# Kernel optimization log

Measured on AMD Instinct MI355X. Metric: run time of the kernel, lower is better.

The kernel has to match this reference:

```python
import jax, jax.numpy as jnp
import numpy as np

H, W = 64, 64          # self.shape = (W, H) = (64, 64)
REG_MAX = 16
TOPK = 4

def _dwconv(y, w, b):
    # y: (N, L, C) -> depthwise 3x3 conv on (N, C, H, W) -> (N, L, C)
    N, L, C = y.shape
    img = jnp.transpose(y, (0, 2, 1)).reshape(N, C, H, W)
    out = jax.lax.conv_general_dilated(
        img, w, (1, 1), ((1, 1), (1, 1)),
        dimension_numbers=('NCHW', 'OIHW', 'NCHW'), feature_group_count=C)
    out = out + b[None, :, None, None]
    return jnp.transpose(out.reshape(N, C, H * W), (0, 2, 1))

def _mlp(x, fc1_w, fc1_b, dw1_w, dw1_b, fc2_w, fc2_b, dw2_w, dw2_b, fc3_w, fc3_b):
    h = x @ fc1_w.T + fc1_b
    h = jax.nn.gelu(_dwconv(h, dw1_w, dw1_b), approximate=False)  # torch nn.GELU is exact erf
    h = h @ fc2_w.T + fc2_b
    h = jax.nn.gelu(_dwconv(h, dw2_w, dw2_b), approximate=False)
    return h @ fc3_w.T + fc3_b

def setup_inputs() -> dict:
    key = jax.random.key(0)
    ks = iter(jax.random.split(key, 16))
    d = {}
    d['x'] = jax.random.normal(next(ks), (1, 32, H * W, 256), dtype=jnp.float32)
    for p in ('c_', 'r_'):
        out3 = 1 if p == 'c_' else 4 * (REG_MAX + 1)
        d[p + 'fc1_w'] = 0.02 * jax.random.normal(next(ks), (256, 256), dtype=jnp.float32)
        d[p + 'fc1_b'] = jnp.zeros((256,), jnp.float32)
        d[p + 'dw1_w'] = 0.3 * jax.random.normal(next(ks), (256, 1, 3, 3), dtype=jnp.float32)
        d[p + 'dw1_b'] = jnp.zeros((256,), jnp.float32)
        d[p + 'fc2_w'] = 0.02 * jax.random.normal(next(ks), (256, 256), dtype=jnp.float32)
        d[p + 'fc2_b'] = jnp.zeros((256,), jnp.float32)
        d[p + 'dw2_w'] = 0.3 * jax.random.normal(next(ks), (256, 1, 3, 3), dtype=jnp.float32)
        d[p + 'dw2_b'] = jnp.zeros((256,), jnp.float32)
        d[p + 'fc3_w'] = 0.02 * jax.random.normal(next(ks), (out3, 256), dtype=jnp.float32)
        d[p + 'fc3_b'] = jnp.zeros((out3,), jnp.float32)
    d['rc1_w'] = 0.1 * jax.random.normal(next(ks), (64, 4 * (TOPK + 1)), dtype=jnp.float32)
    d['rc1_b'] = jnp.zeros((64,), jnp.float32)
    d['rc2_w'] = 0.1 * jax.random.normal(next(ks), (1, 64), dtype=jnp.float32)
    d['rc2_b'] = jnp.zeros((1,), jnp.float32)
    return d

def reference(x,
              c_fc1_w, c_fc1_b, c_dw1_w, c_dw1_b, c_fc2_w, c_fc2_b, c_dw2_w, c_dw2_b, c_fc3_w, c_fc3_b,
              r_fc1_w, r_fc1_b, r_dw1_w, r_dw1_b, r_fc2_w, r_fc2_b, r_dw2_w, r_dw2_b, r_fc3_w, r_fc3_b,
              rc1_w, rc1_b, rc2_w, rc2_b):
    xs = x[0]                                   # (N, L, C)
    N = xs.shape[0]
    reg_pred = _mlp(xs, r_fc1_w, r_fc1_b, r_dw1_w, r_dw1_b, r_fc2_w, r_fc2_b,
                    r_dw2_w, r_dw2_b, r_fc3_w, r_fc3_b)  # (N, L, 4*(reg_max+1))
    prob = jax.nn.softmax(
        jnp.transpose(reg_pred, (0, 2, 1)).reshape(N, 4, REG_MAX + 1, H, W), axis=2)
    pt = jnp.transpose(prob, (0, 1, 3, 4, 2))   # (N,4,H,W,reg_max+1)
    topk, _ = jax.lax.top_k(pt, TOPK)           # (N,4,H,W,topk), sorted desc like torch
    stat = jnp.concatenate([topk, topk.mean(axis=-1, keepdims=True)], axis=-1)
    stat = jnp.transpose(stat, (0, 1, 4, 2, 3)).reshape(N, 4 * (TOPK + 1), H, W)
    q = jax.nn.relu(jnp.einsum('nchw,oc->nohw', stat, rc1_w) + rc1_b[None, :, None, None])
    q = jax.nn.sigmoid(jnp.einsum('nchw,oc->nohw', q, rc2_w) + rc2_b[None, :, None, None])
    cls = _mlp(xs, c_fc1_w, c_fc1_b, c_dw1_w, c_dw1_b, c_fc2_w, c_fc2_b,
               c_dw2_w, c_dw2_b, c_fc3_w, c_fc3_b)      # (N, L, 1)
    cls = jax.nn.sigmoid(jnp.transpose(cls, (0, 2, 1)).reshape(N, 1, H, W)) * q
    proj = jnp.arange(REG_MAX + 1, dtype=reg_pred.dtype)  # linspace(0, reg_max, reg_max+1)
    dist = jax.nn.softmax(reg_pred.reshape(-1, REG_MAX + 1), axis=1) @ proj
    boxes = dist.reshape(N, H, W, 4) / REG_MAX
    return cls, boxes, reg_pred.reshape(N, H, W, 4 * (REG_MAX + 1))
```

## Files before the change

### kernel.cpp

```cpp
#include <hip/hip_runtime.h>
#include <hip/hip_bf16.h>

typedef __bf16 bf16x8 __attribute__((ext_vector_type(8)));
typedef float f32x4 __attribute__((ext_vector_type(4)));
typedef float f32x2 __attribute__((ext_vector_type(2)));

__device__ __forceinline__ float bf2f(unsigned short b) {
  unsigned int u = ((unsigned int)b) << 16;
  return __builtin_bit_cast(float, u);
}
__device__ __forceinline__ unsigned short f2bf(float f) {
  unsigned int u = __builtin_bit_cast(unsigned int, f);
  unsigned int r = u + 0x7fffu + ((u >> 16) & 1u);
  return (unsigned short)(r >> 16);
}
__device__ __forceinline__ f32x2 unpack2(unsigned int u) {
  f32x2 r;
  r.x = __builtin_bit_cast(float, u << 16);
  r.y = __builtin_bit_cast(float, u & 0xffff0000u);
  return r;
}

__device__ __forceinline__ void gload16(const void* g, void* l) {
  typedef __attribute__((address_space(1))) const void* gp_t;
  typedef __attribute__((address_space(3))) void* lp_t;
  __builtin_amdgcn_global_load_lds((gp_t)g, (lp_t)l, 16, 0, 0);
}

__device__ __forceinline__ f32x2 gelu2(f32x2 x) {
  f32x2 m = x * x;
  f32x2 t = m * (-0.10295273f) + (-2.3021967f);
  f32x2 u = x * t;
  f32x2 e;
  e.x = __builtin_amdgcn_exp2f(u.x);
  e.y = __builtin_amdgcn_exp2f(u.y);
  f32x2 d = e + 1.0f;
  f32x2 r;
  r.x = __builtin_amdgcn_rcpf(d.x);
  r.y = __builtin_amdgcn_rcpf(d.y);
  return x * r;
}
__device__ __forceinline__ unsigned int cvt_pk_bf16(float lo, float hi) {
  unsigned int r;
  asm("v_cvt_pk_bf16_f32 %0, %1, %2" : "=v"(r) : "v"(lo), "v"(hi));
  return r;
}

__global__ __launch_bounds__(256) void cvt_x(const float* __restrict__ in,
                                             unsigned short* __restrict__ out) {
  long i = ((long)blockIdx.x * 256 + threadIdx.x) * 8;
  float4 a = *(const float4*)(in + i);
  float4 b = *(const float4*)(in + i + 4);
  __align__(16) unsigned short o[8];
  o[0] = f2bf(a.x); o[1] = f2bf(a.y); o[2] = f2bf(a.z); o[3] = f2bf(a.w);
  o[4] = f2bf(b.x); o[5] = f2bf(b.y); o[6] = f2bf(b.z); o[7] = f2bf(b.w);
  *(uint4*)(out + i) = *(uint4*)o;
}

__global__ __launch_bounds__(256) void prep_all(
    const float* __restrict__ c1w, const float* __restrict__ r1w,
    const float* __restrict__ c2w, const float* __restrict__ r2w,
    const float* __restrict__ c3w, const float* __restrict__ r3w, const float* __restrict__ r3b,
    const float* __restrict__ c1b, const float* __restrict__ r1b,
    const float* __restrict__ c2b, const float* __restrict__ r2b,
    const float* __restrict__ d1wc, const float* __restrict__ d1bc,
    const float* __restrict__ d1wr, const float* __restrict__ d1br,
    const float* __restrict__ d2wc, const float* __restrict__ d2bc,
    const float* __restrict__ d2wr, const float* __restrict__ d2br,
    unsigned short* __restrict__ w1cat, unsigned short* __restrict__ w2cat,
    unsigned short* __restrict__ c3wb, unsigned short* __restrict__ wr3pad,
    float* __restrict__ br3pad, float* __restrict__ b1cat, float* __restrict__ b2cat,
    float* __restrict__ wd1, float* __restrict__ bd1,
    float* __restrict__ wd2, float* __restrict__ bd2) {
  int i = blockIdx.x * 256 + threadIdx.x;
  {
    int which = i >> 16, j = i & 65535;
    float v = (which == 0) ? c1w[j] : (which == 1) ? r1w[j] : (which == 2) ? c2w[j] : r2w[j];
    unsigned short* dst = (which < 2) ? (w1cat + which * 65536) : (w2cat + (which - 2) * 65536);
    dst[j] = f2bf(v);
  }
  if (i < 32768) {
    int r = i >> 8, c = i & 255;
    wr3pad[i] = (r < 68) ? f2bf(r3w[r * 256 + c]) : (unsigned short)0;
    if (i < 128) br3pad[i] = (i < 68) ? r3b[i] : 0.f;
  }
  if (i < 256) c3wb[i] = f2bf(c3w[i]);
  if (i < 4608) {
    int tap = i >> 9, ch = i & 511, cc = ch & 255;
    wd1[i] = (ch < 256) ? d1wc[cc * 9 + tap] : d1wr[cc * 9 + tap];
    wd2[i] = (ch < 256) ? d2wc[cc * 9 + tap] : d2wr[cc * 9 + tap];
  }
  if (i < 512) {
    bd1[i] = (i < 256) ? d1bc[i] : d1br[i & 255];
    bd2[i] = (i < 256) ? d2bc[i] : d2br[i & 255];
    b1cat[i] = (i < 256) ? c1b[i] : r1b[i & 255];
    b2cat[i] = (i < 256) ? c2b[i] : r2b[i & 255];
  }
}

__global__ __launch_bounds__(256, 4) void gemm_glds(
    const unsigned short* __restrict__ A, int lda, int zAoff,
    const unsigned short* __restrict__ W, int zWoff,
    const float* __restrict__ bias, int zBoff,
    unsigned short* __restrict__ Out, int ldo, int zOoff, int lnN,
    float* __restrict__ OutF) {
  __shared__ unsigned short lds[2][8192];
  const int z = blockIdx.z;
  const unsigned short* Az = A + (long)z * zAoff;
  const unsigned short* Wz = W + (long)z * zWoff;
  const float* biasz = bias + z * zBoff;
  unsigned short* Outz = Out + (long)z * zOoff;

  const int nwg = gridDim.x;
  const int bid = blockIdx.x;
  const int wg = (bid & 7) * (nwg >> 3) + (bid >> 3);
  const int mtile = wg >> lnN;
  const int ntile = wg & ((1 << lnN) - 1);
  const long row0 = (long)mtile * 128;
  const int col0 = ntile * 128;

  const int tid = threadIdx.x;
  const int lane = tid & 63;
  const int wid = tid >> 6;
  const int wr = (wid >> 1) * 64;
  const int wc = (wid & 1) * 64;
  const int rr = lane & 15;
  const int gk = lane >> 4;
  const int swz = (rr >> 1) & 3;

  const int srow_l = (wid << 4) + (lane >> 2);
  const int sgl = lane & 3;

  f32x4 acc[4][4] = {};

  auto stage = [&](int buf, int k0) {
    #pragma unroll
    for (int j = 0; j < 4; j++) {
      const int slotbase = j * 256 + (wid << 6);
      unsigned short* ldst = &lds[buf][slotbase * 8];
      const int row = (j & 1) * 64 + srow_l;
      const int g = sgl ^ ((row >> 1) & 3);
      const unsigned short* src;
      if (j < 2) src = Az + (row0 + row) * (long)lda + k0 + g * 8;
      else       src = Wz + (long)(col0 + row) * 256 + k0 + g * 8;
      gload16(src, ldst);
    }
  };

  stage(0, 0);
  #pragma unroll
  for (int ks = 0; ks < 8; ks++) {
    if (ks < 7) {
      stage((ks + 1) & 1, (ks + 1) * 32);
      asm volatile("s_waitcnt vmcnt(4)" ::: "memory");
    } else {
      asm volatile("s_waitcnt vmcnt(0)" ::: "memory");
    }
    __builtin_amdgcn_s_barrier();
    asm volatile("" ::: "memory");
    const unsigned short* buf = lds[ks & 1];
    bf16x8 af[4], bf[4];
    #pragma unroll
    for (int mi = 0; mi < 4; mi++)
      af[mi] = __builtin_bit_cast(bf16x8,
          *(const uint4*)&buf[(wr + mi * 16 + rr) * 32 + ((gk ^ swz) * 8)]);
    #pragma unroll
    for (int ni = 0; ni < 4; ni++)
      bf[ni] = __builtin_bit_cast(bf16x8,
          *(const uint4*)&buf[4096 + (wc + ni * 16 + rr) * 32 + ((gk ^ swz) * 8)]);
    #pragma unroll
    for (int mi = 0; mi < 4; mi++)
      #pragma unroll
      for (int ni = 0; ni < 4; ni++)
        acc[mi][ni] = __builtin_amdgcn_mfma_f32_16x16x32_bf16(af[mi], bf[ni], acc[mi][ni], 0, 0, 0);
    asm volatile("" ::: "memory");
    __builtin_amdgcn_s_barrier();
  }

  #pragma unroll
  for (int mi = 0; mi < 4; mi++) {
    const int rbase = wr + mi * 16 + (lane >> 4) * 4;
    #pragma unroll
    for (int ni = 0; ni < 4; ni++) {
      const int c_ = wc + ni * 16 + (lane & 15);
      const float bv = biasz[col0 + c_];
      #pragma unroll
      for (int r = 0; r < 4; r++) {
        const float val = acc[mi][ni][r] + bv;
        Outz[(row0 + rbase + r) * (long)ldo + col0 + c_] = f2bf(val);
        if (OutF != nullptr && c_ < 68)
          OutF[(row0 + rbase + r) * 68L + c_] = val;
      }
    }
  }
}

template <bool CLS>
__global__ __launch_bounds__(256) void dwconv_gelu4(
    const unsigned short* __restrict__ In,
    const float* __restrict__ Wt, const float* __restrict__ Bt,
    unsigned short* __restrict__ Out,
    const unsigned short* __restrict__ Wc3, const float* __restrict__ bc3,
    float* __restrict__ cls_logit) {
  const int t = blockIdx.x * 256 + threadIdx.x;
  const int g = t & 63;
  const int p = t >> 6;
  const int n = p >> 10;
  const int h = (p >> 4) & 63;
  const int w0 = (p & 15) << 2;
  const int cbase = g << 3;
  f32x2 acc[4][4];
  {
    float4 b0 = *(const float4*)(Bt + cbase);
    float4 b1 = *(const float4*)(Bt + cbase + 4);
    f32x2 bb[4];
    bb[0].x = b0.x; bb[0].y = b0.y; bb[1].x = b0.z; bb[1].y = b0.w;
    bb[2].x = b1.x; bb[2].y = b1.y; bb[3].x = b1.z; bb[3].y = b1.w;
    #pragma unroll
    for (int k = 0; k < 4; k++)
      #pragma unroll
      for (int i = 0; i < 4; i++) acc[k][i] = bb[i];
  }
  #pragma unroll
  for (int dy = -1; dy <= 1; dy++) {
    const int hh = h + dy;
    if (hh < 0 || hh > 63) continue;
    const float* wbase = Wt + ((dy + 1) * 3) * 512 + cbase;
    f32x2 wt[3][4];
    #pragma unroll
    for (int j = 0; j < 3; j++) {
      float4 a0 = *(const float4*)(wbase + j * 512);
      float4 a1 = *(const float4*)(wbase + j * 512 + 4);
      wt[j][0].x = a0.x; wt[j][0].y = a0.y; wt[j][1].x = a0.z; wt[j][1].y = a0.w;
      wt[j][2].x = a1.x; wt[j][2].y = a1.y; wt[j][3].x = a1.z; wt[j][3].y = a1.w;
    }
    const long rowtok = (long)(((n << 6) + hh) << 6);
    f32x2 f[6][4];
    #pragma unroll
    for (int d = 0; d < 6; d++) {
      const int col = w0 - 1 + d;
      uint4 v = {0u, 0u, 0u, 0u};
      if (col >= 0 && col < 64)
        v = *(const uint4*)(In + (rowtok + col) * 512 + cbase);
      f[d][0] = unpack2(v.x); f[d][1] = unpack2(v.y);
      f[d][2] = unpack2(v.z); f[d][3] = unpack2(v.w);
    }
    #pragma unroll
    for (int k = 0; k < 4; k++)
      #pragma unroll
      for (int j = 0; j < 3; j++)
        #pragma unroll
        for (int i = 0; i < 4; i++)
          acc[k][i] += f[k + j][i] * wt[j][i];
  }
  f32x2 w3[4];
  if (CLS) {
    const int cc = cbase & 255;
    uint4 wv = *(const uint4*)(Wc3 + cc);
    w3[0] = unpack2(wv.x); w3[1] = unpack2(wv.y);
    w3[2] = unpack2(wv.z); w3[3] = unpack2(wv.w);
  }
  const long mbase = ((long)((n << 6) + h) << 6) + w0;
  float s[4];
  #pragma unroll
  for (int k = 0; k < 4; k++) {
    __align__(16) unsigned int ov[4];
    f32x2 ge[4];
    #pragma unroll
    for (int i = 0; i < 4; i++) {
      ge[i] = gelu2(acc[k][i]);
      ov[i] = cvt_pk_bf16(ge[i].x, ge[i].y);
    }
    if (!CLS || cbase >= 256)
      *(uint4*)(Out + (mbase + k) * 512 + cbase) = *(uint4*)ov;
    if (CLS) {
      f32x2 sp = ge[0] * w3[0] + ge[1] * w3[1] + ge[2] * w3[2] + ge[3] * w3[3];
      s[k] = sp.x + sp.y;
    }
  }
  if (CLS) {
    #pragma unroll
    for (int k = 0; k < 4; k++) {
      #pragma unroll
      for (int m = 16; m >= 1; m >>= 1) s[k] += __shfl_xor(s[k], m);
    }
    if (g == 0) {
      float b = bc3[0];
      float4 o;
      o.x = s[0] + b; o.y = s[1] + b; o.z = s[2] + b; o.w = s[3] + b;
      *(float4*)(cls_logit + mbase) = o;
    }
  }
}

__global__ __launch_bounds__(256) void post_kernel(
    const unsigned short* __restrict__ RP,
    const float* __restrict__ cls_logit,
    const float* __restrict__ rc1_w, const float* __restrict__ rc1_b,
    const float* __restrict__ rc2_w, const float* __restrict__ rc2_b,
    float* __restrict__ out_cls, float* __restrict__ out_boxes) {
  int m = blockIdx.x * 256 + threadIdx.x;
  const unsigned short* rp = RP + (long)m * 128;
  __align__(16) unsigned short raw[72];
  #pragma unroll
  for (int q = 0; q < 9; q++)
    *(uint4*)(raw + q * 8) = *(const uint4*)(rp + q * 8);
  float stat[20];
  float4 boxes;
  #pragma unroll
  for (int s = 0; s < 4; s++) {
    float v[17];
    float mx = -1e30f;
    #pragma unroll
    for (int i = 0; i < 17; i++) {
      v[i] = bf2f(raw[s * 17 + i]);
      mx = fmaxf(mx, v[i]);
    }
    float sum = 0.f;
    #pragma unroll
    for (int i = 0; i < 17; i++) { v[i] = __expf(v[i] - mx); sum += v[i]; }
    float inv = 1.f / sum;
    float dist = 0.f;
    #pragma unroll
    for (int i = 0; i < 17; i++) { v[i] *= inv; dist += v[i] * (float)i; }
    ((float*)&boxes)[s] = dist * 0.0625f;
    float tk[4];
    #pragma unroll
    for (int t = 0; t < 4; t++) {
      float bm = v[0]; int bi = 0;
      #pragma unroll
      for (int i = 1; i < 17; i++) {
        if (v[i] > bm) { bm = v[i]; bi = i; }
      }
      tk[t] = bm;
      #pragma unroll
      for (int i = 0; i < 17; i++)
        if (i == bi) v[i] = -1.f;
    }
    stat[s * 5 + 0] = tk[0]; stat[s * 5 + 1] = tk[1];
    stat[s * 5 + 2] = tk[2]; stat[s * 5 + 3] = tk[3];
    stat[s * 5 + 4] = 0.25f * (tk[0] + tk[1] + tk[2] + tk[3]);
  }
  *(float4*)(out_boxes + (long)m * 4) = boxes;
  float z = 0.f;
  #pragma unroll
  for (int o = 0; o < 64; o++) {
    float q = rc1_b[o];
    #pragma unroll
    for (int c = 0; c < 20; c++) q += rc1_w[o * 20 + c] * stat[c];
    q = fmaxf(q, 0.f);
    z += q * rc2_w[o];
  }
  z += rc2_b[0];
  float q2 = 1.f / (1.f + __expf(-z));
  float cl = 1.f / (1.f + __expf(-cls_logit[m]));
  out_cls[m] = cl * q2;
}

extern "C" void kernel_launch(void* const* d_in, const int* in_sizes, int n_in,
                              void* d_out, int out_size, void* d_ws, size_t ws_size,
                              hipStream_t stream) {
  const float* x       = (const float*)d_in[0];
  const float* c_fc1_w = (const float*)d_in[1];
  const float* c_fc1_b = (const float*)d_in[2];
  const float* c_dw1_w = (const float*)d_in[3];
  const float* c_dw1_b = (const float*)d_in[4];
  const float* c_fc2_w = (const float*)d_in[5];
  const float* c_fc2_b = (const float*)d_in[6];
  const float* c_dw2_w = (const float*)d_in[7];
  const float* c_dw2_b = (const float*)d_in[8];
  const float* c_fc3_w = (const float*)d_in[9];
  const float* c_fc3_b = (const float*)d_in[10];
  const float* r_fc1_w = (const float*)d_in[11];
  const float* r_fc1_b = (const float*)d_in[12];
  const float* r_dw1_w = (const float*)d_in[13];
  const float* r_dw1_b = (const float*)d_in[14];
  const float* r_fc2_w = (const float*)d_in[15];
  const float* r_fc2_b = (const float*)d_in[16];
  const float* r_dw2_w = (const float*)d_in[17];
  const float* r_dw2_b = (const float*)d_in[18];
  const float* r_fc3_w = (const float*)d_in[19];
  const float* r_fc3_b = (const float*)d_in[20];
  const float* rc1_w   = (const float*)d_in[21];
  const float* rc1_b   = (const float*)d_in[22];
  const float* rc2_w   = (const float*)d_in[23];
  const float* rc2_b   = (const float*)d_in[24];

  char* ws = (char*)d_ws;
  unsigned short* Hbuf = (unsigned short*)ws;
  unsigned short* Gbuf = (unsigned short*)(ws + 134217728L);
  unsigned short* xb   = Gbuf;
  unsigned short* RP   = (unsigned short*)(ws + 268435456L);
  float* cls_logit     = (float*)(ws + 301989888L);
  char* wb             = ws + 302514176L;
  unsigned short* w1cat  = (unsigned short*)wb;
  unsigned short* w2cat  = w1cat + 131072;
  unsigned short* c3wb   = w2cat + 131072;
  unsigned short* wr3pad = c3wb + 256;
  float* br3pad = (float*)(wr3pad + 32768);
  float* b1cat  = br3pad + 128;
  float* b2cat  = b1cat + 512;
  float* wd1    = b2cat + 512;
  float* bd1    = wd1 + 4608;
  float* wd2    = bd1 + 512;
  float* bd2    = wd2 + 4608;

  float* out_cls   = (float*)d_out;
  float* out_boxes = out_cls + 131072;
  float* out_reg   = out_boxes + 524288;

  prep_all<<<1024, 256, 0, stream>>>(
      c_fc1_w, r_fc1_w, c_fc2_w, r_fc2_w, c_fc3_w, r_fc3_w, r_fc3_b,
      c_fc1_b, r_fc1_b, c_fc2_b, r_fc2_b,
      c_dw1_w, c_dw1_b, r_dw1_w, r_dw1_b,
      c_dw2_w, c_dw2_b, r_dw2_w, r_dw2_b,
      w1cat, w2cat, c3wb, wr3pad, br3pad, b1cat, b2cat,
      wd1, bd1, wd2, bd2);
  cvt_x<<<16384, 256, 0, stream>>>(x, xb);

  gemm_glds<<<dim3(4096, 1, 1), 256, 0, stream>>>(
      xb, 256, 0, w1cat, 0, b1cat, 0, Hbuf, 512, 0, 2, nullptr);
  dwconv_gelu4<false><<<8192, 256, 0, stream>>>(Hbuf, wd1, bd1, Gbuf,
                                                nullptr, nullptr, nullptr);
  gemm_glds<<<dim3(2048, 1, 2), 256, 0, stream>>>(
      Gbuf, 512, 256, w2cat, 65536, b2cat, 256, Hbuf, 512, 256, 1, nullptr);
  dwconv_gelu4<true><<<8192, 256, 0, stream>>>(Hbuf, wd2, bd2, Gbuf,
                                               c3wb, c_fc3_b, cls_logit);
  gemm_glds<<<dim3(1024, 1, 1), 256, 0, stream>>>(
      Gbuf + 256, 512, 0, wr3pad, 0, br3pad, 0, RP, 128, 0, 0, out_reg);
  post_kernel<<<512, 256, 0, stream>>>(RP, cls_logit, rc1_w, rc1_b, rc2_w, rc2_b,
                                       out_cls, out_boxes);
}
```

Measured before the change: 344.8 us.

## Fuse regression post-processing into the final GEMM epilogue via LDS staging

```diff
diff --git a/kernel.cpp b/kernel.cpp
--- a/kernel.cpp
+++ b/kernel.cpp
@@ -98,13 +98,19 @@
   }
 }
 
-__global__ __launch_bounds__(256, 4) void gemm_glds(
+template <bool POST>
+__global__ __launch_bounds__(256, 3) void gemm_glds(
     const unsigned short* __restrict__ A, int lda, int zAoff,
     const unsigned short* __restrict__ W, int zWoff,
     const float* __restrict__ bias, int zBoff,
     unsigned short* __restrict__ Out, int ldo, int zOoff, int lnN,
-    float* __restrict__ OutF) {
+    float* __restrict__ OutF,
+    const float* __restrict__ rc1_w, const float* __restrict__ rc1_b,
+    const float* __restrict__ rc2_w, const float* __restrict__ rc2_b,
+    const float* __restrict__ cls_logit,
+    float* __restrict__ out_cls, float* __restrict__ out_boxes) {
   __shared__ unsigned short lds[2][8192];
+  __shared__ float postbuf[POST ? 9344 : 1];
   const int z = blockIdx.z;
   const unsigned short* Az = A + (long)z * zAoff;
   const unsigned short* Wz = W + (long)z * zWoff;
@@ -187,10 +193,71 @@
       #pragma unroll
       for (int r = 0; r < 4; r++) {
         const float val = acc[mi][ni][r] + bv;
-        Outz[(row0 + rbase + r) * (long)ldo + col0 + c_] = f2bf(val);
-        if (OutF != nullptr && c_ < 68)
+        if (!POST) {
+          Outz[(row0 + rbase + r) * (long)ldo + col0 + c_] = f2bf(val);
+        } else if (c_ < 68) {
           OutF[(row0 + rbase + r) * 68L + c_] = val;
+          postbuf[(rbase + r) * 73 + c_] = val;
+        }
       }
+    }
+  }
+
+  if (POST) {
+    __syncthreads();
+    if (tid < 128) {
+      const long m = row0 + tid;
+      const float* pv = postbuf + tid * 73;
+      float stat[20];
+      float4 boxes;
+      #pragma unroll
+      for (int s = 0; s < 4; s++) {
+        float v[17];
+        float mx = -1e30f;
+        #pragma unroll
+        for (int i = 0; i < 17; i++) {
+          v[i] = pv[s * 17 + i];
+          mx = fmaxf(mx, v[i]);
+        }
+        float sum = 0.f;
+        #pragma unroll
+        for (int i = 0; i < 17; i++) { v[i] = __expf(v[i] - mx); sum += v[i]; }
+        float inv = 1.f / sum;
+        float dist = 0.f;
+        #pragma unroll
+        for (int i = 0; i < 17; i++) { v[i] *= inv; dist += v[i] * (float)i; }
+        ((float*)&boxes)[s] = dist * 0.0625f;
+        float tk[4];
+        #pragma unroll
+        for (int t = 0; t < 4; t++) {
+          float bm = v[0]; int bi = 0;
+          #pragma unroll
+          for (int i = 1; i < 17; i++) {
+            if (v[i] > bm) { bm = v[i]; bi = i; }
+          }
+          tk[t] = bm;
+          #pragma unroll
+          for (int i = 0; i < 17; i++)
+            if (i == bi) v[i] = -1.f;
+        }
+        stat[s * 5 + 0] = tk[0]; stat[s * 5 + 1] = tk[1];
+        stat[s * 5 + 2] = tk[2]; stat[s * 5 + 3] = tk[3];
+        stat[s * 5 + 4] = 0.25f * (tk[0] + tk[1] + tk[2] + tk[3]);
+      }
+      *(float4*)(out_boxes + m * 4) = boxes;
+      float zz = 0.f;
+      #pragma unroll
+      for (int o = 0; o < 64; o++) {
+        float q = rc1_b[o];
+        #pragma unroll
+        for (int c = 0; c < 20; c++) q += rc1_w[o * 20 + c] * stat[c];
+        q = fmaxf(q, 0.f);
+        zz += q * rc2_w[o];
+      }
+      zz += rc2_b[0];
+      float q2 = 1.f / (1.f + __expf(-zz));
+      float cl = 1.f / (1.f + __expf(-cls_logit[m]));
+      out_cls[m] = cl * q2;
     }
   }
 }
@@ -291,70 +358,6 @@
       *(float4*)(cls_logit + mbase) = o;
     }
   }
-}
-
-__global__ __launch_bounds__(256) void post_kernel(
-    const unsigned short* __restrict__ RP,
-    const float* __restrict__ cls_logit,
-    const float* __restrict__ rc1_w, const float* __restrict__ rc1_b,
-    const float* __restrict__ rc2_w, const float* __restrict__ rc2_b,
-    float* __restrict__ out_cls, float* __restrict__ out_boxes) {
-  int m = blockIdx.x * 256 + threadIdx.x;
-  const unsigned short* rp = RP + (long)m * 128;
-  __align__(16) unsigned short raw[72];
-  #pragma unroll
-  for (int q = 0; q < 9; q++)
-    *(uint4*)(raw + q * 8) = *(const uint4*)(rp + q * 8);
-  float stat[20];
-  float4 boxes;
-  #pragma unroll
-  for (int s = 0; s < 4; s++) {
-    float v[17];
-    float mx = -1e30f;
-    #pragma unroll
-    for (int i = 0; i < 17; i++) {
-      v[i] = bf2f(raw[s * 17 + i]);
-      mx = fmaxf(mx, v[i]);
-    }
-    float sum = 0.f;
-    #pragma unroll
-    for (int i = 0; i < 17; i++) { v[i] = __expf(v[i] - mx); sum += v[i]; }
-    float inv = 1.f / sum;
-    float dist = 0.f;
-    #pragma unroll
-    for (int i = 0; i < 17; i++) { v[i] *= inv; dist += v[i] * (float)i; }
-    ((float*)&boxes)[s] = dist * 0.0625f;
-    float tk[4];
-    #pragma unroll
-    for (int t = 0; t < 4; t++) {
-      float bm = v[0]; int bi = 0;
-      #pragma unroll
-      for (int i = 1; i < 17; i++) {
-        if (v[i] > bm) { bm = v[i]; bi = i; }
-      }
-      tk[t] = bm;
-      #pragma unroll
-      for (int i = 0; i < 17; i++)
-        if (i == bi) v[i] = -1.f;
-    }
-    stat[s * 5 + 0] = tk[0]; stat[s * 5 + 1] = tk[1];
-    stat[s * 5 + 2] = tk[2]; stat[s * 5 + 3] = tk[3];
-    stat[s * 5 + 4] = 0.25f * (tk[0] + tk[1] + tk[2] + tk[3]);
-  }
-  *(float4*)(out_boxes + (long)m * 4) = boxes;
-  float z = 0.f;
-  #pragma unroll
-  for (int o = 0; o < 64; o++) {
-    float q = rc1_b[o];
-    #pragma unroll
-    for (int c = 0; c < 20; c++) q += rc1_w[o * 20 + c] * stat[c];
-    q = fmaxf(q, 0.f);
-    z += q * rc2_w[o];
-  }
-  z += rc2_b[0];
-  float q2 = 1.f / (1.f + __expf(-z));
-  float cl = 1.f / (1.f + __expf(-cls_logit[m]));
-  out_cls[m] = cl * q2;
 }
 
 extern "C" void kernel_launch(void* const* d_in, const int* in_sizes, int n_in,
@@ -390,9 +393,8 @@
   unsigned short* Hbuf = (unsigned short*)ws;
   unsigned short* Gbuf = (unsigned short*)(ws + 134217728L);
   unsigned short* xb   = Gbuf;
-  unsigned short* RP   = (unsigned short*)(ws + 268435456L);
-  float* cls_logit     = (float*)(ws + 301989888L);
-  char* wb             = ws + 302514176L;
+  float* cls_logit     = (float*)(ws + 268435456L);
+  char* wb             = ws + 268959744L;
   unsigned short* w1cat  = (unsigned short*)wb;
   unsigned short* w2cat  = w1cat + 131072;
   unsigned short* c3wb   = w2cat + 131072;
@@ -418,16 +420,17 @@
       wd1, bd1, wd2, bd2);
   cvt_x<<<16384, 256, 0, stream>>>(x, xb);
 
-  gemm_glds<<<dim3(4096, 1, 1), 256, 0, stream>>>(
-      xb, 256, 0, w1cat, 0, b1cat, 0, Hbuf, 512, 0, 2, nullptr);
+  gemm_glds<false><<<dim3(4096, 1, 1), 256, 0, stream>>>(
+      xb, 256, 0, w1cat, 0, b1cat, 0, Hbuf, 512, 0, 2, nullptr,
+      nullptr, nullptr, nullptr, nullptr, nullptr, nullptr, nullptr);
   dwconv_gelu4<false><<<8192, 256, 0, stream>>>(Hbuf, wd1, bd1, Gbuf,
                                                 nullptr, nullptr, nullptr);
-  gemm_glds<<<dim3(2048, 1, 2), 256, 0, stream>>>(
-      Gbuf, 512, 256, w2cat, 65536, b2cat, 256, Hbuf, 512, 256, 1, nullptr);
+  gemm_glds<false><<<dim3(2048, 1, 2), 256, 0, stream>>>(
+      Gbuf, 512, 256, w2cat, 65536, b2cat, 256, Hbuf, 512, 256, 1, nullptr,
+      nullptr, nullptr, nullptr, nullptr, nullptr, nullptr, nullptr);
   dwconv_gelu4<true><<<8192, 256, 0, stream>>>(Hbuf, wd2, bd2, Gbuf,
                                                c3wb, c_fc3_b, cls_logit);
-  gemm_glds<<<dim3(1024, 1, 1), 256, 0, stream>>>(
-      Gbuf + 256, 512, 0, wr3pad, 0, br3pad, 0, RP, 128, 0, 0, out_reg);
-  post_kernel<<<512, 256, 0, stream>>>(RP, cls_logit, rc1_w, rc1_b, rc2_w, rc2_b,
-                                       out_cls, out_boxes);
-}
+  gemm_glds<true><<<dim3(1024, 1, 1), 256, 0, stream>>>(
+      Gbuf + 256, 512, 0, wr3pad, 0, br3pad, 0, nullptr, 128, 0, 0, out_reg,
+      rc1_w, rc1_b, rc2_w, rc2_b, cls_logit, out_cls, out_boxes);
+}
```

Result: no change. 345.1 us (+0.1%).
